# Kernel optimization log

Measured on AMD Instinct MI355X. Metric: run time of the kernel, lower is better.

Reference implementation:

```python
import jax, jax.numpy as jnp
import numpy as np

N = 50000      # nodes
E = 800000     # edges (avg degree 16)
H = 256        # h_size
MAXCTX = 8     # max_context


def setup_inputs() -> dict:
    key = jax.random.key(0)
    ks = jax.random.split(key, 6)
    x = jax.random.normal(ks[0], (N, H), jnp.float32)
    edge_index = jax.random.randint(ks[1], (2, E), 0, N)
    node_label = jax.random.randint(ks[2], (N, MAXCTX), 0, N)
    context_len = jax.random.randint(ks[3], (N,), 0, MAXCTX)
    gcn_W = jax.random.normal(ks[4], (H, H), jnp.float32) / np.sqrt(H)
    gcn_b = jnp.zeros((H,), jnp.float32)
    resize_W = jax.random.normal(ks[5], (H * MAXCTX, H), jnp.float32) / np.sqrt(H * MAXCTX)
    resize_b = jnp.zeros((H,), jnp.float32)
    return {"x": x, "edge_index": edge_index, "node_label": node_label,
            "context_len": context_len, "gcn_W": gcn_W, "gcn_b": gcn_b,
            "resize_W": resize_W, "resize_b": resize_b}


def gcn_conv(x, edge_index, W, b, n):
    # PyG GCNConv: add self-loops, symmetric deg^-1/2 normalization, then linear.
    loop = jnp.arange(n)
    src = jnp.concatenate([edge_index[0], loop])
    dst = jnp.concatenate([edge_index[1], loop])
    deg = jax.ops.segment_sum(jnp.ones_like(dst, x.dtype), dst, num_segments=n)
    inv_sqrt = jax.lax.rsqrt(jnp.maximum(deg, 1.0))  # deg>=1 due to self-loops
    h = x @ W                                        # [n, H]
    coef = inv_sqrt[src] * inv_sqrt[dst]             # [E+n]
    out = jax.ops.segment_sum(h[src] * coef[:, None], dst, num_segments=n)
    return out + b


def reference(x, edge_index, node_label, context_len, gcn_W, gcn_b, resize_W, resize_b):
    n = x.shape[0]
    # gcn_layers=2: relu(GCN(x)) (dropout is identity in eval) then GCN again.
    feat = jax.nn.relu(gcn_conv(x, edge_index, gcn_W, gcn_b, n))
    feat = gcn_conv(feat, edge_index, gcn_W, gcn_b, n)
    # Batched variable-length context gather with zero padding.
    ctx = feat[node_label]                                            # [n, MAXCTX, H]
    mask = (jnp.arange(node_label.shape[1])[None, :] < context_len[:, None])
    ctx = ctx * mask[:, :, None].astype(feat.dtype)
    ctx = ctx.reshape(n, -1) @ resize_W + resize_b                    # [n, H]
    return feat * ctx                                                 # rep_vec per node
```

## Files before the change

### kernel.cpp

```cpp
#include <hip/hip_runtime.h>

typedef _Float16 f16;
typedef _Float16 f16x8 __attribute__((ext_vector_type(8)));
typedef float f32x16 __attribute__((ext_vector_type(16)));

#define MFMA(a, b, c) __builtin_amdgcn_mfma_f32_32x32x16_f16(a, b, c, 0, 0, 0)

__device__ __forceinline__ void gload_lds16(const f16* g, f16* l) {
    __builtin_amdgcn_global_load_lds(
        (const __attribute__((address_space(1))) unsigned int*)g,
        (__attribute__((address_space(3))) unsigned int*)l, 16, 0, 0);
}


#define NBMAX 256
#define CHUNK 8192
#define CAP   8192

__global__ __launch_bounds__(256) void bin_count_trans(
        const int* __restrict__ dst, const int* __restrict__ clen,
        int* __restrict__ gbc, int* __restrict__ ghist, int E, int n, int chn,
        int nbc,
        const float* __restrict__ gW, f16* __restrict__ Wth, f16* __restrict__ Wtl,
        const float* __restrict__ rW, f16* __restrict__ Rth, f16* __restrict__ Rtl) {
    __shared__ int bc[NBMAX];
    __shared__ int ch[9];
    __shared__ f16 Th[64][68], Tl[64][68];
    int tid = threadIdx.x;
    if ((int)blockIdx.x >= nbc) {
        int b = (int)blockIdx.x - nbc;
        const float* src; f16 *dh, *dl; int K, k0, n0;
        if (b < 128) { src = rW; dh = Rth; dl = Rtl; K = 2048; k0 = (b >> 2) * 64; n0 = (b & 3) * 64; }
        else { int bb = b - 128; src = gW; dh = Wth; dl = Wtl; K = 256; k0 = (bb >> 2) * 64; n0 = (bb & 3) * 64; }
        int c = tid & 63, r0 = tid >> 6;
        for (int rr = r0; rr < 64; rr += 4) {
            float v = src[(size_t)(k0 + rr) * 256 + n0 + c];
            f16 h = (f16)v;
            Th[rr][c] = h; Tl[rr][c] = (f16)(v - (float)h);
        }
        __syncthreads();
        int k = tid & 63, nr0 = tid >> 6;
        for (int nn = nr0; nn < 64; nn += 4) {
            size_t oidx = (size_t)(n0 + nn) * K + k0 + k;
            dh[oidx] = Th[k][nn];
            dl[oidx] = Tl[k][nn];
        }
        return;
    }
    bc[tid] = 0;
    if (tid < 9) ch[tid] = 0;
    __syncthreads();
    int e0 = blockIdx.x * CHUNK, e1 = min(e0 + CHUNK, E);
    for (int i = e0 + tid; i < e1; i += 256)
        atomicAdd(&bc[dst[i] >> 8], 1);
    int n0 = blockIdx.x * chn, n1 = min(n0 + chn, n);
    for (int i = n0 + tid; i < n1; i += 256) {
        int l = clen[i]; l = max(0, min(8, l));
        atomicAdd(&ch[l], 1);
    }
    __syncthreads();
    if (bc[tid]) atomicAdd(&gbc[tid], bc[tid]);
    if (tid < 9 && ch[tid]) atomicAdd(&ghist[tid], ch[tid]);
}

__global__ __launch_bounds__(256) void scan_small(
        const int* __restrict__ gbc, int* __restrict__ gbase,
        const int* __restrict__ ghist, int* __restrict__ chbase, int nb, int E) {
    __shared__ int s[NBMAX];
    int tid = threadIdx.x;
    int v = (tid < nb) ? gbc[tid] : 0;
    s[tid] = v;
    __syncthreads();
    for (int off = 1; off < 256; off <<= 1) {
        int u = (tid >= off) ? s[tid - off] : 0;
        __syncthreads();
        s[tid] += u;
        __syncthreads();
    }
    if (tid <= nb) gbase[tid] = (tid < nb) ? s[tid] - v : E;
    if (tid == 0) {
        int run = 0;
        for (int i = 0; i < 9; ++i) { int c = ghist[i]; chbase[i] = run; run += c; }
    }
}

__global__ __launch_bounds__(256) void bin_scatter(
        const int* __restrict__ src, const int* __restrict__ dst,
        const int* __restrict__ clen,
        const int* __restrict__ gbase, int* __restrict__ gfill,
        const int* __restrict__ chbase, int* __restrict__ chfill,
        int2* __restrict__ binned, int* __restrict__ perm, int* __restrict__ plen,
        int E, int n, int chn) {
    __shared__ int bc[NBMAX], bb[NBMAX];
    __shared__ int cc[9], cb[9];
    int tid = threadIdx.x;
    bc[tid] = 0;
    if (tid < 9) cc[tid] = 0;
    __syncthreads();
    int e0 = blockIdx.x * CHUNK, e1 = min(e0 + CHUNK, E);
    for (int i = e0 + tid; i < e1; i += 256)
        atomicAdd(&bc[dst[i] >> 8], 1);
    int n0 = blockIdx.x * chn, n1 = min(n0 + chn, n);
    for (int i = n0 + tid; i < n1; i += 256) {
        int l = clen[i]; l = max(0, min(8, l));
        atomicAdd(&cc[l], 1);
    }
    __syncthreads();
    {
        int c = bc[tid];
        bb[tid] = c ? gbase[tid] + atomicAdd(&gfill[tid], c) : 0;
        bc[tid] = 0;
    }
    if (tid < 9) {
        int c = cc[tid];
        cb[tid] = c ? chbase[tid] + atomicAdd(&chfill[tid], c) : 0;
        cc[tid] = 0;
    }
    __syncthreads();
    for (int i = e0 + tid; i < e1; i += 256) {
        int d = dst[i], b = d >> 8;
        int p = bb[b] + atomicAdd(&bc[b], 1);
        binned[p] = make_int2(src[i], d);
    }
    for (int i = n0 + tid; i < n1; i += 256) {
        int l = clen[i]; l = max(0, min(8, l));
        int p = cb[l] + atomicAdd(&cc[l], 1);
        perm[p] = i;
        plen[p] = l;
    }
}

__global__ __launch_bounds__(256) void csr_build(
        const int2* __restrict__ binned, const int* __restrict__ gbase,
        int* __restrict__ row_ptr, float* __restrict__ inv_s,
        int* __restrict__ ew, int E, int n) {
    __shared__ int cnt[256], base[256], fill[256];
    __shared__ int ebuf[CAP];
    int tid = threadIdx.x, b = blockIdx.x;
    int e0 = gbase[b], e1 = gbase[b + 1], sz = e1 - e0;
    cnt[tid] = 0;
    __syncthreads();
    for (int i = e0 + tid; i < e1; i += 256)
        atomicAdd(&cnt[binned[i].y & 255], 1);
    __syncthreads();
    int v = cnt[tid];
    base[tid] = v;
    __syncthreads();
    for (int off = 1; off < 256; off <<= 1) {
        int u = (tid >= off) ? base[tid - off] : 0;
        __syncthreads();
        base[tid] += u;
        __syncthreads();
    }
    int ex = base[tid] - v;
    base[tid] = ex;
    fill[tid] = 0;
    int node = b * 256 + tid;
    if (node < n) {
        row_ptr[node] = e0 + ex;
        inv_s[node] = rsqrtf((float)(v + 1));
    }
    if (b == 0 && tid == 0) row_ptr[n] = E;
    __syncthreads();
    for (int i = e0 + tid; i < e1; i += 256) {
        int2 q = binned[i];
        int lo = q.y & 255;
        int p = base[lo] + atomicAdd(&fill[lo], 1);
        if (p < CAP) ebuf[p] = q.x; else ew[e0 + p] = q.x;
    }
    __syncthreads();
    int lim = min(sz, CAP);
    for (int p = tid; p < lim; p += 256) ew[e0 + p] = ebuf[p];
}


union H4 { f16 f[4]; ushort4 u; };

__global__ __launch_bounds__(512, 4) void agg_split(const float* __restrict__ X,
        const int* __restrict__ ew, const int* __restrict__ rp,
        const float* __restrict__ invs, f16* __restrict__ ohi, f16* __restrict__ olo, int n) {
    __shared__ float part[4][256];
    int w = threadIdx.x >> 6, lane = threadIdx.x & 63;
    int local = w >> 1, half = w & 1;
    int node = blockIdx.x * 4 + local;
    bool active = node < n;
    float4 acc = make_float4(0.f, 0.f, 0.f, 0.f);
    float si = 0.f;
    if (active) {
        si = invs[node];
        int e0 = rp[node], e1 = rp[node + 1];
        int mid = e0 + ((e1 - e0 + 1) >> 1);
        int lo = half ? mid : e0;
        int hi = half ? e1 : mid;
        if (!half) {
            float4 a = *((const float4*)(X + (size_t)node * 256) + lane);
            acc = make_float4(a.x * si, a.y * si, a.z * si, a.w * si);
        }
        int e = lo;
        for (; e + 8 <= hi; e += 8) {
            int q[8]; float ws[8]; float4 v[8];
            #pragma unroll
            for (int u = 0; u < 8; ++u) q[u] = ew[e + u];
            #pragma unroll
            for (int u = 0; u < 8; ++u) ws[u] = invs[q[u]];
            #pragma unroll
            for (int u = 0; u < 8; ++u) v[u] = *((const float4*)(X + (size_t)q[u] * 256) + lane);
            #pragma unroll
            for (int u = 0; u < 8; ++u) {
                acc.x = fmaf(ws[u], v[u].x, acc.x); acc.y = fmaf(ws[u], v[u].y, acc.y);
                acc.z = fmaf(ws[u], v[u].z, acc.z); acc.w = fmaf(ws[u], v[u].w, acc.w);
            }
        }
        for (; e < hi; ++e) {
            int q = ew[e];
            float wq = invs[q];
            float4 v = *((const float4*)(X + (size_t)q * 256) + lane);
            acc.x = fmaf(wq, v.x, acc.x); acc.y = fmaf(wq, v.y, acc.y);
            acc.z = fmaf(wq, v.z, acc.z); acc.w = fmaf(wq, v.w, acc.w);
        }
    }
    if (half) *(float4*)&part[local][lane * 4] = acc;
    __syncthreads();
    if (!half && active) {
        float4 o = *(const float4*)&part[local][lane * 4];
        float v0 = si * (acc.x + o.x), v1 = si * (acc.y + o.y);
        float v2 = si * (acc.z + o.z), v3 = si * (acc.w + o.w);
        H4 hh, ll;
        f16 h;
        h = (f16)v0; hh.f[0] = h; ll.f[0] = (f16)(v0 - (float)h);
        h = (f16)v1; hh.f[1] = h; ll.f[1] = (f16)(v1 - (float)h);
        h = (f16)v2; hh.f[2] = h; ll.f[2] = (f16)(v2 - (float)h);
        h = (f16)v3; hh.f[3] = h; ll.f[3] = (f16)(v3 - (float)h);
        size_t off = (size_t)node * 256 + lane * 4;
        *(ushort4*)(ohi + off) = hh.u;
        *(ushort4*)(olo + off) = ll.u;
    }
}


__global__ __launch_bounds__(256, 3) void gemm_lds(
        const f16* __restrict__ Ahi, const f16* __restrict__ Alo,
        const f16* __restrict__ Wth, const f16* __restrict__ Wtl,
        const float* __restrict__ bias,
        float* __restrict__ Of32, f16* __restrict__ Ohi, f16* __restrict__ Olo,
        int M, int relu) {
    __shared__ __align__(16) f16 LA[3][2][4096];
    int tid = threadIdx.x, w = tid >> 6, lane = tid & 63;
    int row0 = (int)blockIdx.x * 64;
    int m = lane & 31, kh = lane >> 5;
    const int T = 4;

    f32x16 acc[2][2] = {};

    {
        #define STAGE(t_, b_)                                                     \
        {                                                                         \
            int k0e_ = (t_) * 64;                                                 \
            int rl_ = lane >> 3;                                                  \
            int k8s_ = (lane & 7) ^ rl_;                                          \
            _Pragma("unroll")                                                     \
            for (int q = 0; q < 4; ++q) {                                         \
                int o_ = w * 4 + q;                                               \
                int mat_ = o_ >> 3, rg_ = o_ & 7;                                 \
                int r_ = row0 + rg_ * 8 + rl_;                                    \
                if (r_ >= M) r_ = M - 1;                                          \
                const f16* base_ = mat_ ? Alo : Ahi;                              \
                const f16* g_ = base_ + (size_t)r_ * 256 + k0e_ + k8s_ * 8;       \
                gload_lds16(g_, &LA[b_][mat_][rg_ * 512]);                        \
            }                                                                     \
        }
        STAGE(0, 0);
        STAGE(1, 1);
        asm volatile("s_waitcnt vmcnt(0)" ::: "memory");
        __builtin_amdgcn_s_barrier();
        __builtin_amdgcn_sched_barrier(0);
        for (int t = 0; t < T; ++t) {
            int b = t % 3;
            int k0e = t * 64;
            f16x8 Bh[4][2], Bl[4][2];
            #pragma unroll
            for (int jt = 0; jt < 2; ++jt) {
                int nn = w * 64 + jt * 32 + m;
                size_t boff = (size_t)nn * 256 + k0e + kh * 8;
                const f16* ph = Wth + boff;
                const f16* pl = Wtl + boff;
                #pragma unroll
                for (int s = 0; s < 4; ++s) {
                    Bh[s][jt] = *(const f16x8*)(ph + s * 16);
                    Bl[s][jt] = *(const f16x8*)(pl + s * 16);
                }
            }
            __builtin_amdgcn_sched_barrier(0);
            if (t + 2 < T) STAGE(t + 2, (t + 2) % 3);
            __builtin_amdgcn_sched_barrier(0);
            #pragma unroll
            for (int s = 0; s < 4; ++s) {
                int k8 = s * 2 + kh;
                int slot = (k8 ^ (m & 7)) * 8;
                f16x8 ah[2], al[2];
                #pragma unroll
                for (int i = 0; i < 2; ++i) {
                    int ro = (i * 32 + m) * 64;
                    ah[i] = *(const f16x8*)&LA[b][0][ro + slot];
                    al[i] = *(const f16x8*)&LA[b][1][ro + slot];
                }
                #pragma unroll
                for (int jt = 0; jt < 2; ++jt) {
                    #pragma unroll
                    for (int i = 0; i < 2; ++i) {
                        acc[i][jt] = MFMA(ah[i], Bh[s][jt], acc[i][jt]);
                        acc[i][jt] = MFMA(ah[i], Bl[s][jt], acc[i][jt]);
                        acc[i][jt] = MFMA(al[i], Bh[s][jt], acc[i][jt]);
                    }
                }
            }
            if (t + 2 < T) {
                asm volatile("s_waitcnt vmcnt(4)" ::: "memory");
            } else {
                asm volatile("s_waitcnt vmcnt(0)" ::: "memory");
            }
            __builtin_amdgcn_s_barrier();
            __builtin_amdgcn_sched_barrier(0);
        }
        #undef STAGE
    }

    #pragma unroll
    for (int jt = 0; jt < 2; ++jt) {
        int col = w * 64 + jt * 32 + m;
        float bv = bias[col];
        #pragma unroll
        for (int i = 0; i < 2; ++i) {
            #pragma unroll
            for (int r = 0; r < 16; ++r) {
                int row = row0 + i * 32 + (r & 3) + 8 * (r >> 2) + 4 * kh;
                if (row < M) {
                    float v = acc[i][jt][r] + bv;
                    if (relu) v = fmaxf(v, 0.f);
                    size_t idx = (size_t)row * 256 + col;
                    if (Of32) Of32[idx] = v;
                    if (Ohi) {
                        f16 h = (f16)v;
                        Ohi[idx] = h; Olo[idx] = (f16)(v - (float)h);
                    }
                }
            }
        }
    }
}


__global__ __launch_bounds__(512) void ctx_gemm(
        const f16* __restrict__ fhi, const f16* __restrict__ flo,
        const int* __restrict__ perm, const int* __restrict__ plen,
        const int* __restrict__ label,
        const f16* __restrict__ Rth, const f16* __restrict__ Rtl,
        const float* __restrict__ rbias, float* __restrict__ out,
        const f16* __restrict__ zp, int M) {
    __shared__ __align__(16) f16 LA[2][2][4096];
    __shared__ int s_lbl[8][64];
    __shared__ int s_perm[64];
    __shared__ int s_max;
    int tid = threadIdx.x, w = tid >> 6, lane = tid & 63;
    int row0 = (int)(gridDim.x - 1 - blockIdx.x) * 64;
    int m = lane & 31, kh = lane >> 5;

    if (tid == 0) s_max = 0;
    __syncthreads();
    if (tid < 64) {
        int r = row0 + tid;
        int p = (r < M) ? perm[r] : -1;
        s_perm[tid] = p;
        int len = (r < M) ? plen[r] : 0;
        atomicMax(&s_max, len);
        int4 l0 = make_int4(-1, -1, -1, -1), l1 = l0;
        if (p >= 0) {
            l0 = *(const int4*)(label + (size_t)p * 8);
            l1 = *(const int4*)(label + (size_t)p * 8 + 4);
        }
        s_lbl[0][tid] = (0 < len) ? l0.x : -1;
        s_lbl[1][tid] = (1 < len) ? l0.y : -1;
        s_lbl[2][tid] = (2 < len) ? l0.z : -1;
        s_lbl[3][tid] = (3 < len) ? l0.w : -1;
        s_lbl[4][tid] = (4 < len) ? l1.x : -1;
        s_lbl[5][tid] = (5 < len) ? l1.y : -1;
        s_lbl[6][tid] = (6 < len) ? l1.z : -1;
        s_lbl[7][tid] = (7 < len) ? l1.w : -1;
    }
    __syncthreads();
    int T = s_max * 4;

    f32x16 acc[2] = {};

    if (T > 0) {
        #define STAGE(t_, b_)                                                     \
        {                                                                         \
            int j_ = (t_) >> 2, k0e_ = ((t_) & 3) * 64;                           \
            int rl_ = lane >> 3;                                                  \
            int k8s_ = (lane & 7) ^ rl_;                                          \
            _Pragma("unroll")                                                     \
            for (int q = 0; q < 2; ++q) {                                         \
                int o_ = w * 2 + q;                                               \
                int mat_ = o_ >> 3, rg_ = o_ & 7;                                 \
                int lbl_ = s_lbl[j_][rg_ * 8 + rl_];                              \
                const f16* base_ = mat_ ? flo : fhi;                              \
                const f16* g_ = (lbl_ >= 0)                                       \
                    ? base_ + (size_t)lbl_ * 256 + k0e_ + k8s_ * 8 : zp;          \
                gload_lds16(g_, &LA[b_][mat_][rg_ * 512]);                        \
            }                                                                     \
        }
        STAGE(0, 0);
        __syncthreads();
        for (int t = 0; t < T; ++t) {
            if (t + 1 < T) STAGE(t + 1, (t + 1) & 1);
            int b = t & 1;
            int j = t >> 2, k0e = (t & 3) * 64;
            int nn = w * 32 + m;
            size_t boff = (size_t)nn * 2048 + j * 256 + k0e + kh * 8;
            const f16* pBh = Rth + boff;
            const f16* pBl = Rtl + boff;
            #pragma unroll
            for (int s = 0; s < 4; ++s) {
                int k8 = s * 2 + kh;
                int slot = (k8 ^ (m & 7)) * 8;
                f16x8 ah[2], al[2];
                #pragma unroll
                for (int i = 0; i < 2; ++i) {
                    int ro = (i * 32 + m) * 64;
                    ah[i] = *(const f16x8*)&LA[b][0][ro + slot];
                    al[i] = *(const f16x8*)&LA[b][1][ro + slot];
                }
                f16x8 bh = *(const f16x8*)(pBh + s * 16);
                f16x8 bl = *(const f16x8*)(pBl + s * 16);
                #pragma unroll
                for (int i = 0; i < 2; ++i) {
                    acc[i] = MFMA(ah[i], bh, acc[i]);
                    acc[i] = MFMA(ah[i], bl, acc[i]);
                    acc[i] = MFMA(al[i], bh, acc[i]);
                }
            }
            __syncthreads();
        }
        #undef STAGE
    }

    {
        int col = w * 32 + m;
        float rbv = rbias[col];
        #pragma unroll
        for (int i = 0; i < 2; ++i) {
            #pragma unroll
            for (int r = 0; r < 16; ++r) {
                int lr = i * 32 + (r & 3) + 8 * (r >> 2) + 4 * kh;
                int p = s_perm[lr];
                if (p >= 0) {
                    size_t idx = (size_t)p * 256 + col;
                    float f2 = (float)fhi[idx] + (float)flo[idx];
                    out[idx] = f2 * (acc[i][r] + rbv);
                }
            }
        }
    }
}


extern "C" void kernel_launch(void* const* d_in, const int* in_sizes, int n_in,
                              void* d_out, int out_size, void* d_ws, size_t ws_size,
                              hipStream_t stream) {
    const float* x    = (const float*)d_in[0];
    const int*   edge = (const int*)d_in[1];
    const int*   lbl  = (const int*)d_in[2];
    const int*   clen = (const int*)d_in[3];
    const float* gW   = (const float*)d_in[4];
    const float* gb   = (const float*)d_in[5];
    const float* rW   = (const float*)d_in[6];
    const float* rb   = (const float*)d_in[7];

    const int N = in_sizes[3];
    const int E = in_sizes[1] / 2;

    char* ws = (char*)d_ws;
    size_t off = 0;
    auto take = [&](size_t bytes) -> char* {
        char* p = ws + off;
        off = (off + bytes + 255) & ~(size_t)255;
        return p;
    };
    int*   g_small  = (int*)take(1024 * sizeof(int));
    int*   g_bcnt   = g_small;
    int*   g_bbase  = g_small + 256;
    int*   g_bfill  = g_small + 520;
    int*   g_chist  = g_small + 776;
    int*   g_chbase = g_small + 792;
    int*   g_chfill = g_small + 808;
    int*   row_ptr = (int*)take((size_t)(N + 1) * sizeof(int));
    int*   ew      = (int*)take((size_t)E * sizeof(int));
    int*   perm    = (int*)take((size_t)N * sizeof(int));
    int*   plen    = (int*)take((size_t)N * sizeof(int));
    float* inv_s   = (float*)take((size_t)N * sizeof(float));
    f16*   zp      = (f16*)take(1024);
    f16*   Wth     = (f16*)take((size_t)256 * 256 * sizeof(f16));
    f16*   Wtl     = (f16*)take((size_t)256 * 256 * sizeof(f16));
    f16*   Rth     = (f16*)take((size_t)256 * 2048 * sizeof(f16));
    f16*   Rtl     = (f16*)take((size_t)256 * 2048 * sizeof(f16));
    f16*   Ahi     = (f16*)take((size_t)N * 256 * sizeof(f16));
    f16*   Alo     = (f16*)take((size_t)N * 256 * sizeof(f16));
    float* Y1      = (float*)take((size_t)N * 256 * sizeof(float));
    f16*   Fhi     = (f16*)take((size_t)N * 256 * sizeof(f16));
    f16*   Flo     = (f16*)take((size_t)N * 256 * sizeof(f16));
    int2*  binned  = (int2*)Y1;

    hipMemsetAsync(g_small, 0, 1024 * sizeof(int), stream);
    hipMemsetAsync(zp, 0, 1024, stream);

    int NB   = (N + 255) >> 8;
    int GBIN = (E + CHUNK - 1) / CHUNK;
    int CHN  = (N + GBIN - 1) / GBIN;

    bin_count_trans<<<GBIN + 144, 256, 0, stream>>>(edge + E, clen, g_bcnt, g_chist,
                                                    E, N, CHN, GBIN,
                                                    gW, Wth, Wtl, rW, Rth, Rtl);
    scan_small<<<1, 256, 0, stream>>>(g_bcnt, g_bbase, g_chist, g_chbase, NB, E);
    bin_scatter<<<GBIN, 256, 0, stream>>>(edge, edge + E, clen, g_bbase, g_bfill,
                                          g_chbase, g_chfill, binned, perm, plen,
                                          E, N, CHN);
    csr_build<<<NB, 256, 0, stream>>>(binned, g_bbase, row_ptr, inv_s, ew, E, N);

    int gB64 = (N + 63) / 64;
    agg_split<<<(N + 3) / 4, 512, 0, stream>>>(x, ew, row_ptr, inv_s, Ahi, Alo, N);
    gemm_lds<<<gB64, 256, 0, stream>>>(Ahi, Alo, Wth, Wtl, gb, Y1, nullptr, nullptr, N, 1);
    agg_split<<<(N + 3) / 4, 512, 0, stream>>>(Y1, ew, row_ptr, inv_s, Ahi, Alo, N);
    gemm_lds<<<gB64, 256, 0, stream>>>(Ahi, Alo, Wth, Wtl, gb, nullptr, Fhi, Flo, N, 0);
    ctx_gemm<<<gB64, 512, 0, stream>>>(Fhi, Flo, perm, plen, lbl, Rth, Rtl,
                                       rb, (float*)d_out, zp, N);
}
```

Measured before the change: 670.7 us.

## Sort nodes by degree for load-balanced aggregation blocks

Builds a degree histogram in csr_build, scans it in descending order, and scatters nodes into a degree-sorted permutation. Both aggregation passes now process nodes in that order, so each block handles nodes of similar degree and wave imbalance drops. The cost is two extra small kernels and an extra indirection. It also gives up the locality of writing consecutive output rows, since each block now writes to scattered nodes.

```diff
diff --git a/kernel.cpp b/kernel.cpp
--- a/kernel.cpp
+++ b/kernel.cpp
@@ -133,7 +133,7 @@
 __global__ __launch_bounds__(256) void csr_build(
         const int2* __restrict__ binned, const int* __restrict__ gbase,
         int* __restrict__ row_ptr, float* __restrict__ inv_s,
-        int* __restrict__ ew, int E, int n) {
+        int* __restrict__ ew, int* __restrict__ dhist, int E, int n) {
     __shared__ int cnt[256], base[256], fill[256];
     __shared__ int ebuf[CAP];
     int tid = threadIdx.x, b = blockIdx.x;
@@ -159,6 +159,7 @@
     if (node < n) {
         row_ptr[node] = e0 + ex;
         inv_s[node] = rsqrtf((float)(v + 1));
+        atomicAdd(&dhist[min(v, 63)], 1);
     }
     if (b == 0 && tid == 0) row_ptr[n] = E;
     __syncthreads();
@@ -173,17 +174,38 @@
     for (int p = tid; p < lim; p += 256) ew[e0 + p] = ebuf[p];
 }
 
+__global__ __launch_bounds__(64) void deg_scan(const int* __restrict__ dhist,
+                                               int* __restrict__ dbase) {
+    if (threadIdx.x == 0) {
+        int run = 0;
+        for (int d = 63; d >= 0; --d) { dbase[d] = run; run += dhist[d]; }
+    }
+}
+
+__global__ __launch_bounds__(256) void deg_scatter(
+        const int* __restrict__ row_ptr, const int* __restrict__ dbase,
+        int* __restrict__ dfill, int* __restrict__ dperm, int n) {
+    int i = blockIdx.x * 256 + threadIdx.x;
+    if (i < n) {
+        int d = min(row_ptr[i + 1] - row_ptr[i], 63);
+        int p = dbase[d] + atomicAdd(&dfill[d], 1);
+        dperm[p] = i;
+    }
+}
+
 
 union H4 { f16 f[4]; ushort4 u; };
 
 __global__ __launch_bounds__(512, 4) void agg_split(const float* __restrict__ X,
         const int* __restrict__ ew, const int* __restrict__ rp,
-        const float* __restrict__ invs, f16* __restrict__ ohi, f16* __restrict__ olo, int n) {
+        const float* __restrict__ invs, const int* __restrict__ dperm,
+        f16* __restrict__ ohi, f16* __restrict__ olo, int n) {
     __shared__ float part[4][256];
     int w = threadIdx.x >> 6, lane = threadIdx.x & 63;
     int local = w >> 1, half = w & 1;
-    int node = blockIdx.x * 4 + local;
-    bool active = node < n;
+    int idx = blockIdx.x * 4 + local;
+    int node = (idx < n) ? dperm[idx] : -1;
+    bool active = node >= 0;
     float4 acc = make_float4(0.f, 0.f, 0.f, 0.f);
     float si = 0.f;
     if (active) {
@@ -493,10 +515,14 @@
     int*   g_chist  = g_small + 776;
     int*   g_chbase = g_small + 792;
     int*   g_chfill = g_small + 808;
+    int*   g_dhist  = g_small + 832;
+    int*   g_dbase  = g_small + 896;
+    int*   g_dfill  = g_small + 960;
     int*   row_ptr = (int*)take((size_t)(N + 1) * sizeof(int));
     int*   ew      = (int*)take((size_t)E * sizeof(int));
     int*   perm    = (int*)take((size_t)N * sizeof(int));
     int*   plen    = (int*)take((size_t)N * sizeof(int));
+    int*   dperm   = (int*)take((size_t)N * sizeof(int));
     float* inv_s   = (float*)take((size_t)N * sizeof(float));
     f16*   zp      = (f16*)take(1024);
     f16*   Wth     = (f16*)take((size_t)256 * 256 * sizeof(f16));
@@ -524,12 +550,14 @@
     bin_scatter<<<GBIN, 256, 0, stream>>>(edge, edge + E, clen, g_bbase, g_bfill,
                                           g_chbase, g_chfill, binned, perm, plen,
                                           E, N, CHN);
-    csr_build<<<NB, 256, 0, stream>>>(binned, g_bbase, row_ptr, inv_s, ew, E, N);
+    csr_build<<<NB, 256, 0, stream>>>(binned, g_bbase, row_ptr, inv_s, ew, g_dhist, E, N);
+    deg_scan<<<1, 64, 0, stream>>>(g_dhist, g_dbase);
+    deg_scatter<<<NB, 256, 0, stream>>>(row_ptr, g_dbase, g_dfill, dperm, N);
 
     int gB64 = (N + 63) / 64;
-    agg_split<<<(N + 3) / 4, 512, 0, stream>>>(x, ew, row_ptr, inv_s, Ahi, Alo, N);
+    agg_split<<<(N + 3) / 4, 512, 0, stream>>>(x, ew, row_ptr, inv_s, dperm, Ahi, Alo, N);
     gemm_lds<<<gB64, 256, 0, stream>>>(Ahi, Alo, Wth, Wtl, gb, Y1, nullptr, nullptr, N, 1);
-    agg_split<<<(N + 3) / 4, 512, 0, stream>>>(Y1, ew, row_ptr, inv_s, Ahi, Alo, N);
+    agg_split<<<(N + 3) / 4, 512, 0, stream>>>(Y1, ew, row_ptr, inv_s, dperm, Ahi, Alo, N);
     gemm_lds<<<gB64, 256, 0, stream>>>(Ahi, Alo, Wth, Wtl, gb, nullptr, Fhi, Flo, N, 0);
     ctx_gemm<<<gB64, 512, 0, stream>>>(Fhi, Flo, perm, plen, lbl, Rth, Rtl,
                                        rb, (float*)d_out, zp, N);
```

Result: slower. 937.5 us (+39.8%).
